# Kernel tuning notes

Measured on AMD Instinct MI355X. Metric: run time of the kernel, lower is better.

The kernel has to match this reference:

```python
import jax, jax.numpy as jnp
import numpy as np

B, H, W, C = 32, 56, 56, 128
HEADS, WS, SHIFT = 4, 7, 3
P = 10            # prompt_len = PERTASK_LEN(5) * n_tasks(2)
R = 4             # LoRA rank
HID = 512         # mlp hidden = 4*C
LORA_SCALE = 1.0
NW = (H // WS) * (W // WS)
NWIN = WS * WS


def _rel_pos_index():
    coords = np.stack(np.meshgrid(np.arange(WS), np.arange(WS), indexing='ij')).reshape(2, -1)
    rel = (coords[:, :, None] - coords[:, None, :]).transpose(1, 2, 0)
    rel[:, :, 0] += WS - 1
    rel[:, :, 1] += WS - 1
    rel[:, :, 0] *= 2 * WS - 1
    return rel.sum(-1)  # (49, 49)


def _attn_mask():
    img = np.zeros((H, W))
    cnt = 0
    for hs in (slice(0, -WS), slice(-WS, -SHIFT), slice(-SHIFT, None)):
        for ws_ in (slice(0, -WS), slice(-WS, -SHIFT), slice(-SHIFT, None)):
            img[hs, ws_] = cnt
            cnt += 1
    mw = img.reshape(H // WS, WS, W // WS, WS).transpose(0, 2, 1, 3).reshape(-1, NWIN)
    am = mw[:, None, :] - mw[:, :, None]
    return np.where(am != 0, -100.0, 0.0).astype(np.float32)  # (nW, 49, 49)

RPI = _rel_pos_index()
ATTN_MASK = jnp.asarray(_attn_mask())


def window_partition(x):  # (B,H,W,C) -> (B*nW, ws*ws, C)
    b = x.shape[0]
    x = x.reshape(b, H // WS, WS, W // WS, WS, C)
    return x.transpose(0, 1, 3, 2, 4, 5).reshape(-1, NWIN, C)


def window_reverse(w):  # (B*nW, ws*ws, C) -> (B,H,W,C)
    x = w.reshape(-1, H // WS, W // WS, WS, WS, C)
    return x.transpose(0, 1, 3, 2, 4, 5).reshape(-1, H, W, C)


def _ln(t, g, b):
    m = t.mean(-1, keepdims=True)
    v = ((t - m) ** 2).mean(-1, keepdims=True)
    return (t - m) / jnp.sqrt(v + 1e-5) * g + b


def _tal(t, w, b, la, lb):  # TAModuleLinear: base linear + shared LoRA branch
    return t @ w + b + (t @ la) @ lb * LORA_SCALE


def setup_inputs() -> dict:
    key = jax.random.key(0)
    ks = jax.random.split(key, 16)
    s = 0.02
    return {
        'x': jax.random.normal(ks[0], (B, H * W, C), jnp.float32),
        'spa_prompts': jax.random.normal(ks[1], (B, P, C), jnp.float32),
        'norm1_g': jnp.ones((C,), jnp.float32),
        'norm1_b': jnp.zeros((C,), jnp.float32),
        'qkv_w': jax.random.normal(ks[2], (C, 3 * C), jnp.float32) * s,
        'qkv_b': jnp.zeros((3 * C,), jnp.float32),
        'qkv_la': jax.random.normal(ks[3], (C, R), jnp.float32) * s,
        'qkv_lb': jax.random.normal(ks[4], (R, 3 * C), jnp.float32) * s,
        'rpb_table': jax.random.normal(ks[5], ((2 * WS - 1) ** 2, HEADS), jnp.float32) * s,
        'proj_w': jax.random.normal(ks[6], (C, C), jnp.float32) * s,
        'proj_b': jnp.zeros((C,), jnp.float32),
        'proj_la': jax.random.normal(ks[7], (C, R), jnp.float32) * s,
        'proj_lb': jax.random.normal(ks[8], (R, C), jnp.float32) * s,
        'norm2_g': jnp.ones((C,), jnp.float32),
        'norm2_b': jnp.zeros((C,), jnp.float32),
        'fc1_w': jax.random.normal(ks[9], (C, HID), jnp.float32) * s,
        'fc1_b': jnp.zeros((HID,), jnp.float32),
        'fc1_la': jax.random.normal(ks[10], (C, R), jnp.float32) * s,
        'fc1_lb': jax.random.normal(ks[11], (R, HID), jnp.float32) * s,
        'fc2_w': jax.random.normal(ks[12], (HID, C), jnp.float32) * s,
        'fc2_b': jnp.zeros((C,), jnp.float32),
        'fc2_la': jax.random.normal(ks[13], (HID, R), jnp.float32) * s,
        'fc2_lb': jax.random.normal(ks[14], (R, C), jnp.float32) * s,
    }


def reference(x, spa_prompts, norm1_g, norm1_b, qkv_w, qkv_b, qkv_la, qkv_lb,
              rpb_table, proj_w, proj_b, proj_la, proj_lb, norm2_g, norm2_b,
              fc1_w, fc1_b, fc1_la, fc1_lb, fc2_w, fc2_b, fc2_la, fc2_lb):
    d = C // HEADS
    qk_scale = d ** -0.5
    N = NWIN + P
    B_ = B * NW

    shortcut = x
    h = _ln(x, norm1_g, norm1_b).reshape(B, H, W, C)
    h = jnp.roll(h, shift=(-SHIFT, -SHIFT), axis=(1, 2))          # cyclic shift
    xw = window_partition(h)                                      # (B*nW, 49, C)

    # prepend shared spatial prompts to every window
    sp = jnp.broadcast_to(spa_prompts[:, None], (B, NW, P, C)).reshape(B_, P, C)
    t = jnp.concatenate([sp, xw], axis=1)                         # (B_, N, C)

    qkv = _tal(t, qkv_w, qkv_b, qkv_la, qkv_lb)
    qkv = qkv.reshape(B_, N, 3, HEADS, d).transpose(2, 0, 3, 1, 4)
    q, k, v = qkv[0], qkv[1], qkv[2]

    attn = jnp.einsum('bhnd,bhmd->bhnm', q, k) * qk_scale         # (B_, h, N, N)
    bias = rpb_table[RPI.reshape(-1)].reshape(NWIN, NWIN, HEADS).transpose(2, 0, 1)
    attn = attn.at[:, :, P:, P:].add(bias[None])
    attn = attn.reshape(B, NW, HEADS, N, N)
    attn = attn.at[:, :, :, P:, P:].add(ATTN_MASK[None, :, None]) # shifted-window mask
    attn = jax.nn.softmax(attn.reshape(B_, HEADS, N, N), axis=-1)

    out = jnp.einsum('bhnm,bhmd->bnhd', attn, v).reshape(B_, N, C)
    out = _tal(out, proj_w, proj_b, proj_la, proj_lb)

    out = out[:, P:]                                              # drop prompt tokens
    h = window_reverse(out)
    h = jnp.roll(h, shift=(SHIFT, SHIFT), axis=(1, 2)).reshape(B, H * W, C)
    x1 = shortcut + h                                             # attn residual

    m = _ln(x1, norm2_g, norm2_b)
    m = jax.nn.gelu(_tal(m, fc1_w, fc1_b, fc1_la, fc1_lb), approximate=False)
    m = _tal(m, fc2_w, fc2_b, fc2_la, fc2_lb)
    return x1 + m
```

## Files before the change

### kernel.cpp

```cpp
#include <hip/hip_runtime.h>

typedef unsigned short u16;
typedef unsigned int   u32;
typedef short bf16x8 __attribute__((ext_vector_type(8)));
typedef short bf16x4 __attribute__((ext_vector_type(4)));
typedef float f32x4  __attribute__((ext_vector_type(4)));

#define HIMG 56
#define WIMG 56
#define CH   128
#define NHEADS 4
#define WSZ  7
#define SSH  3
#define PP   10
#define HIDD 512
#define NWIN 49
#define NTOK 59
#define BWIN 2048
#define DH   32
#define MWIN 120832
#define MPIX 100352

__device__ __forceinline__ u16 f2b(float f) {
  u32 u = __float_as_uint(f);
  u += 0x7fffu + ((u >> 16) & 1u);
  return (u16)(u >> 16);
}
__device__ __forceinline__ u32 pack2(float a, float b) {
  return (u32)f2b(a) | ((u32)f2b(b) << 16);
}
__device__ __forceinline__ float gelu(float x) {
  const float z = fabsf(x) * 0.70710678118654752f;
  const float t = 1.0f / (1.0f + 0.3275911f * z);
  const float p = t * (0.254829592f + t * (-0.284496736f + t * (1.421413741f +
                  t * (-1.453152027f + t * 1.061405429f))));
  const float erfz = copysignf(1.0f - p * __expf(-z * z), x);
  return 0.5f * x * (1.0f + erfz);
}

__global__ void fuse_all_kernel(
    const float* __restrict__ qw,  const float* __restrict__ qa,  const float* __restrict__ qb,
    const float* __restrict__ pw,  const float* __restrict__ pa,  const float* __restrict__ pb,
    const float* __restrict__ f1w, const float* __restrict__ f1a, const float* __restrict__ f1b,
    const float* __restrict__ f2w, const float* __restrict__ f2a, const float* __restrict__ f2b2,
    u16* __restrict__ out)
{
  int idx = blockIdx.x * 256 + threadIdx.x;
  if (idx >= 196608) return;
  int n, k, Nc;
  const float *w, *la, *lb;
  if (idx < 49152) {
    const int li = idx;
    const int j = li & 7, lane = (li >> 3) & 63, kk = (li >> 9) & 3, c16 = li >> 11;
    n = c16 * 16 + (lane & 15);
    k = kk * 32 + (lane >> 4) * 8 + j;
    w = qw; la = qa; lb = qb; Nc = 384;
  } else if (idx < 65536) {
    const int li = idx - 49152;
    const int j = li & 7, lane = (li >> 3) & 63, kk = (li >> 9) & 3, c16 = li >> 11;
    n = c16 * 16 + (lane & 15);
    k = kk * 32 + (lane >> 4) * 8 + j;
    w = pw; la = pa; lb = pb; Nc = 128;
  } else if (idx < 131072) {
    const int li = idx - 65536;
    const int j = li & 7, lane = (li >> 3) & 63, kk = (li >> 9) & 3, c16 = li >> 11;
    n = c16 * 16 + (lane & 15);
    k = kk * 32 + (lane >> 4) * 8 + j;
    w = f1w; la = f1a; lb = f1b; Nc = 512;
  } else {
    const int li = idx - 131072;
    const int j = li & 7, lane = (li >> 3) & 63, kk2 = (li >> 9) & 1, hb = (li >> 10) & 7, o16 = li >> 13;
    n = o16 * 16 + (lane & 15);
    k = hb * 64 + kk2 * 32 + (lane >> 4) * 8 + j;
    w = f2w; la = f2a; lb = f2b2; Nc = 128;
  }
  float s = w[k * Nc + n];
  #pragma unroll
  for (int r = 0; r < 4; ++r) s += la[k * 4 + r] * lb[r * Nc + n];
  out[idx] = f2b(s);
}

__global__ void bm_kernel(const float* __restrict__ rpb, float* __restrict__ bm)
{
  const int idx = blockIdx.x * 256 + threadIdx.x;
  const int j = idx & 63, i = (idx >> 6) & 63, h = (idx >> 12) & 3, type = idx >> 14;
  float v = 0.f;
  if (i < 49) {
    if (j >= 59) v = -1e30f;
    else if (j >= PP) {
      const int jw = j - PP;
      const int ih = i / 7, iw = i - ih * 7, jh = jw / 7, jw2 = jw - jh * 7;
      v = rpb[((ih - jh + 6) * 13 + (iw - jw2 + 6)) * NHEADS + h];
      const int wh7 = type >> 1, ww7 = type & 1;
      const int mi = 3 * (wh7 ? (ih < 4 ? 1 : 2) : 0) + (ww7 ? (iw < 4 ? 1 : 2) : 0);
      const int mj = 3 * (wh7 ? (jh < 4 ? 1 : 2) : 0) + (ww7 ? (jw2 < 4 ? 1 : 2) : 0);
      if (mi != mj) v -= 100.f;
    }
  }
  bm[idx] = v;
}

__global__ __launch_bounds__(256) void ln1_gather_kernel(
    const float* __restrict__ x, const float* __restrict__ prompts,
    const float* __restrict__ g, const float* __restrict__ bb,
    u16* __restrict__ t)
{
  const int tok  = blockIdx.x * 4 + (threadIdx.x >> 6);
  const int lane = threadIdx.x & 63;
  const int b_ = tok / NTOK, n = tok - b_ * NTOK;
  u32* dst = (u32*)(t + (size_t)tok * CH) + lane;
  if (n < PP) {
    const int b = b_ >> 6;
    const float2 v = *(const float2*)(prompts + ((size_t)b * PP + n) * CH + lane * 2);
    *dst = pack2(v.x, v.y);
    return;
  }
  const int w  = b_ & 63;
  const int wi = n - PP;
  const int hr = (w >> 3) * WSZ + wi / WSZ;
  const int wc = (w & 7) * WSZ + wi % WSZ;
  const int hs  = (hr + SSH) % HIMG;
  const int ws2 = (wc + SSH) % WIMG;
  const float2 v = *(const float2*)(x + ((size_t)(b_ >> 6) * (HIMG * WIMG) + hs * WIMG + ws2) * CH + lane * 2);
  float s = v.x + v.y, s2 = v.x * v.x + v.y * v.y;
  #pragma unroll
  for (int o = 32; o > 0; o >>= 1) { s += __shfl_xor(s, o); s2 += __shfl_xor(s2, o); }
  const float mean = s * (1.0f / CH);
  const float inv  = rsqrtf(s2 * (1.0f / CH) - mean * mean + 1e-5f);
  const float2 gg = *(const float2*)(g  + lane * 2);
  const float2 bv = *(const float2*)(bb + lane * 2);
  *dst = pack2((v.x - mean) * inv * gg.x + bv.x, (v.y - mean) * inv * gg.y + bv.y);
}

#define QKS 136
#define VTS 72
#define PS  68
__global__ __launch_bounds__(256, 3) void qkv_attn_kernel(
    const u16* __restrict__ t, const u16* __restrict__ wqf,
    const float* __restrict__ qbias, const float* __restrict__ bm,
    u16* __restrict__ attn_out)
{
  __shared__ __align__(16) u16 smem[26624];
  u16* q_lds = smem;
  u16* k_lds = smem + 64 * QKS;
  u16* vt    = smem + 128 * QKS;
  u16* p_lds = smem;

  const int tid = threadIdx.x;
  const int wv = tid >> 6, lane = tid & 63;
  const int lr = lane & 15, lk = lane >> 4;
  const int b_ = blockIdx.x;
  const long tbase = (long)b_ * NTOK;

  bf16x8 af[4][4];
  #pragma unroll
  for (int mt = 0; mt < 4; ++mt) {
    int tok = mt * 16 + lr; if (tok > 58) tok = 58;
    #pragma unroll
    for (int kk = 0; kk < 4; ++kk)
      af[mt][kk] = *(const bf16x8*)(t + (tbase + tok) * CH + kk * 32 + lk * 8);
  }
  #pragma unroll
  for (int nf = 0; nf < 6; ++nf) {
    const int c = wv * 96 + nf * 16 + lr;
    const int sel = wv * 6 + nf;
    bf16x8 bw[4];
    #pragma unroll
    for (int kk = 0; kk < 4; ++kk)
      bw[kk] = *(const bf16x8*)(wqf + ((sel * 4 + kk) * 64 + lane) * 8);
    f32x4 a4[4];
    #pragma unroll
    for (int mt = 0; mt < 4; ++mt) a4[mt] = (f32x4){0.f, 0.f, 0.f, 0.f};
    #pragma unroll
    for (int kk = 0; kk < 4; ++kk)
      #pragma unroll
      for (int mt = 0; mt < 4; ++mt)
        a4[mt] = __builtin_amdgcn_mfma_f32_16x16x32_bf16(af[mt][kk], bw[kk], a4[mt], 0, 0, 0);
    const float bs = qbias[c];
    #pragma unroll
    for (int mt = 0; mt < 4; ++mt) {
      const int tok0 = mt * 16 + lk * 4;
      if (sel < 8) {
        #pragma unroll
        for (int rg = 0; rg < 4; ++rg)
          q_lds[(tok0 + rg) * QKS + c] = f2b(a4[mt][rg] + bs);
      } else if (sel < 16) {
        #pragma unroll
        for (int rg = 0; rg < 4; ++rg)
          k_lds[(tok0 + rg) * QKS + (c - 128)] = f2b(a4[mt][rg] + bs);
      } else {
        ushort4 pk = make_ushort4(f2b(a4[mt][0] + bs), f2b(a4[mt][1] + bs),
                                  f2b(a4[mt][2] + bs), f2b(a4[mt][3] + bs));
        *(ushort4*)&vt[(c - 256) * VTS + tok0] = pk;
      }
    }
  }
  __syncthreads();

  const int h = wv;
  const int w = b_ & 63;
  const int type = (((w >> 3) == 7) ? 2 : 0) + (((w & 7) == 7) ? 1 : 0);
  const float scale = 0.17677669529663687f;

  bf16x8 kf[4], qf[4];
  #pragma unroll
  for (int t4 = 0; t4 < 4; ++t4) {
    kf[t4] = *(const bf16x8*)&k_lds[(t4 * 16 + lr) * QKS + h * DH + lk * 8];
    int tq = PP + t4 * 16 + lr; if (tq > 63) tq = 63;
    qf[t4] = *(const bf16x8*)&q_lds[tq * QKS + h * DH + lk * 8];
  }
  f32x4 sacc[4][4];
  #pragma unroll
  for (int a = 0; a < 4; ++a)
    #pragma unroll
    for (int b = 0; b < 4; ++b)
      sacc[a][b] = (f32x4){0.f, 0.f, 0.f, 0.f};
  #pragma unroll
  for (int mtj = 0; mtj < 4; ++mtj)
    #pragma unroll
    for (int nti = 0; nti < 4; ++nti)
      sacc[mtj][nti] = __builtin_amdgcn_mfma_f32_16x16x32_bf16(kf[mtj], qf[nti], sacc[mtj][nti], 0, 0, 0);

  const float* bmh = bm + (size_t)(type * NHEADS + h) * 64 * 64;
  #pragma unroll
  for (int nti = 0; nti < 4; ++nti) {
    const int i = nti * 16 + lr;
    float sv[16];
    #pragma unroll
    for (int mtj = 0; mtj < 4; ++mtj) {
      const float4 bmv = *(const float4*)(bmh + i * 64 + mtj * 16 + lk * 4);
      sv[mtj * 4 + 0] = sacc[mtj][nti][0] * scale + bmv.x;
      sv[mtj * 4 + 1] = sacc[mtj][nti][1] * scale + bmv.y;
      sv[mtj * 4 + 2] = sacc[mtj][nti][2] * scale + bmv.z;
      sv[mtj * 4 + 3] = sacc[mtj][nti][3] * scale + bmv.w;
    }
    float mx = sv[0];
    #pragma unroll
    for (int q = 1; q < 16; ++q) mx = fmaxf(mx, sv[q]);
    mx = fmaxf(mx, __shfl_xor(mx, 16));
    mx = fmaxf(mx, __shfl_xor(mx, 32));
    float sum = 0.f;
    #pragma unroll
    for (int q = 0; q < 16; ++q) { sv[q] = __expf(sv[q] - mx); sum += sv[q]; }
    sum += __shfl_xor(sum, 16);
    sum += __shfl_xor(sum, 32);
    const float inv = 1.0f / sum;
    #pragma unroll
    for (int mtj = 0; mtj < 4; ++mtj) {
      sacc[mtj][nti][0] = sv[mtj * 4 + 0] * inv;
      sacc[mtj][nti][1] = sv[mtj * 4 + 1] * inv;
      sacc[mtj][nti][2] = sv[mtj * 4 + 2] * inv;
      sacc[mtj][nti][3] = sv[mtj * 4 + 3] * inv;
    }
  }
  __syncthreads();

  u16* ph = p_lds + h * 64 * PS;
  #pragma unroll
  for (int nti = 0; nti < 4; ++nti) {
    const int i = nti * 16 + lr;
    #pragma unroll
    for (int mtj = 0; mtj < 4; ++mtj) {
      const ushort4 pk = make_ushort4(f2b(sacc[mtj][nti][0]), f2b(sacc[mtj][nti][1]),
                                      f2b(sacc[mtj][nti][2]), f2b(sacc[mtj][nti][3]));
      *(ushort4*)&ph[i * PS + mtj * 16 + lk * 4] = pk;
    }
  }
  __syncthreads();

  f32x4 oacc[4][2];
  #pragma unroll
  for (int a = 0; a < 4; ++a) { oacc[a][0] = (f32x4){0,0,0,0}; oacc[a][1] = (f32x4){0,0,0,0}; }
  #pragma unroll
  for (int ks = 0; ks < 2; ++ks) {
    bf16x8 pa[4];
    #pragma unroll
    for (int mt = 0; mt < 4; ++mt) {
      const u16* pr = &ph[(mt * 16 + lr) * PS + ks * 32 + lk * 8];
      const bf16x4 lo = *(const bf16x4*)pr;
      const bf16x4 hi = *(const bf16x4*)(pr + 4);
      pa[mt] = __builtin_shufflevector(lo, hi, 0, 1, 2, 3, 4, 5, 6, 7);
    }
    bf16x8 bv[2];
    #pragma unroll
    for (int nd = 0; nd < 2; ++nd)
      bv[nd] = *(const bf16x8*)&vt[(h * DH + nd * 16 + lr) * VTS + ks * 32 + lk * 8];
    #pragma unroll
    for (int mt = 0; mt < 4; ++mt)
      #pragma unroll
      for (int nd = 0; nd < 2; ++nd)
        oacc[mt][nd] = __builtin_amdgcn_mfma_f32_16x16x32_bf16(pa[mt], bv[nd], oacc[mt][nd], 0, 0, 0);
  }

  #pragma unroll
  for (int mt = 0; mt < 4; ++mt)
    #pragma unroll
    for (int rg = 0; rg < 4; ++rg) {
      const int i = mt * 16 + lk * 4 + rg;
      ph[i * PS + lr]      = f2b(oacc[mt][0][rg]);
      ph[i * PS + 16 + lr] = f2b(oacc[mt][1][rg]);
    }
  __syncthreads();
  if (lane < NWIN) {
    const u16* src = &ph[lane * PS];
    u16* dst = attn_out + ((size_t)b_ * NWIN + lane) * CH + h * DH;
    #pragma unroll
    for (int c = 0; c < 8; ++c)
      *(uint2*)(dst + c * 4) = *(const uint2*)(src + c * 4);
  }
}

#define HS 68
__global__ __launch_bounds__(256, 4) void proj_mlp_kernel(
    const u16* __restrict__ ao, const u16* __restrict__ wprojf,
    const float* __restrict__ pbias, const float* __restrict__ x,
    const float* __restrict__ g2, const float* __restrict__ b2,
    const u16* __restrict__ w1f, const float* __restrict__ b1,
    const u16* __restrict__ w2f, const float* __restrict__ b2f,
    float* __restrict__ outp)
{
  __shared__ __align__(16) char smem[33792];
  u16*   sa  = (u16*)smem;
  float* T32 = (float*)smem;
  u16*   sm  = (u16*)(smem + 16896);
  u16*   H   = (u16*)(smem + 25088);
  const int tid = threadIdx.x;
  const int wv = tid >> 6, lane = tid & 63;
  const int lr = lane & 15, lk = lane >> 4;
  const long rowbase = (long)blockIdx.x * 32;

  #pragma unroll
  for (int it = 0; it < 2; ++it) {
    const int c = it * 256 + tid;
    const int r = c >> 4, s = c & 15;
    const int k8 = s ^ (r & 15);
    const int pix = (int)rowbase + r;
    const int b  = pix / 3136;
    const int rem = pix - b * 3136;
    const int hf = rem / 56, wf = rem - hf * 56;
    int hs = hf + 53; if (hs >= 56) hs -= 56;
    int ws2 = wf + 53; if (ws2 >= 56) ws2 -= 56;
    const int w  = (hs / 7) * 8 + (ws2 / 7);
    const int wi = (hs % 7) * 7 + (ws2 % 7);
    const long arow = ((long)b * 64 + w) * NWIN + wi;
    __builtin_amdgcn_global_load_lds((const void*)(ao + arow * CH + k8 * 8),
                                     (void*)(sa + c * 8), 16, 0, 0);
  }
  __syncthreads();

  f32x4 pacc[2][2];
  #pragma unroll
  for (int a = 0; a < 2; ++a) { pacc[a][0] = (f32x4){0,0,0,0}; pacc[a][1] = (f32x4){0,0,0,0}; }
  #pragma unroll
  for (int kk = 0; kk < 4; ++kk) {
    bf16x8 af[2];
    #pragma unroll
    for (int mt = 0; mt < 2; ++mt) {
      const int r = mt * 16 + lr;
      af[mt] = *(const bf16x8*)(sa + r * 128 + (((kk * 4 + lk) ^ (r & 15)) << 3));
    }
    #pragma unroll
    for (int nf = 0; nf < 2; ++nf) {
      const int c16 = wv * 2 + nf;
      const bf16x8 bw = *(const bf16x8*)(wprojf + ((c16 * 4 + kk) * 64 + lane) * 8);
      #pragma unroll
      for (int mt = 0; mt < 2; ++mt)
        pacc[mt][nf] = __builtin_amdgcn_mfma_f32_16x16x32_bf16(af[mt], bw, pacc[mt][nf], 0, 0, 0);
    }
  }
  __syncthreads();

  #pragma unroll
  for (int nf = 0; nf < 2; ++nf) {
    const int col = (wv * 2 + nf) * 16 + lr;
    const float bs = pbias[col];
    #pragma unroll
    for (int mt = 0; mt < 2; ++mt)
      #pragma unroll
      for (int j = 0; j < 4; ++j)
        T32[(mt * 16 + lk * 4 + j) * 132 + col] = pacc[mt][nf][j] + bs;
  }
  __syncthreads();
  const int rl = tid >> 3, q = tid & 7;
  float4 xv[4];
  float sum = 0.f, sq = 0.f;
  {
    const float* xrow = x + (rowbase + rl) * CH;
    #pragma unroll
    for (int i = 0; i < 4; ++i) {
      float4 tv = *(const float4*)&T32[rl * 132 + q * 4 + i * 32];
      const float4 xr = *(const float4*)(xrow + q * 4 + i * 32);
      tv.x += xr.x; tv.y += xr.y; tv.z += xr.z; tv.w += xr.w;
      xv[i] = tv;
      sum += tv.x + tv.y + tv.z + tv.w;
      sq  += tv.x * tv.x + tv.y * tv.y + tv.z * tv.z + tv.w * tv.w;
    }
  }
  sum += __shfl_xor(sum, 1); sq += __shfl_xor(sq, 1);
  sum += __shfl_xor(sum, 2); sq += __shfl_xor(sq, 2);
  sum += __shfl_xor(sum, 4); sq += __shfl_xor(sq, 4);
  {
    const float mean = sum * (1.0f / CH);
    const float inv  = rsqrtf(sq * (1.0f / CH) - mean * mean + 1e-5f);
    #pragma unroll
    for (int i = 0; i < 4; ++i) {
      const int col0 = q * 4 + i * 32;
      const float4 gg = *(const float4*)(g2 + col0);
      const float4 bb = *(const float4*)(b2 + col0);
      const float m0 = (xv[i].x - mean) * inv * gg.x + bb.x;
      const float m1 = (xv[i].y - mean) * inv * gg.y + bb.y;
      const float m2 = (xv[i].z - mean) * inv * gg.z + bb.z;
      const float m3 = (xv[i].w - mean) * inv * gg.w + bb.w;
      const int slot = col0 >> 3;
      const int off = rl * 128 + ((slot ^ (rl & 15)) << 3) + (col0 & 7);
      uint2 pk; pk.x = pack2(m0, m1); pk.y = pack2(m2, m3);
      *(uint2*)&sm[off] = pk;
    }
  }
  __syncthreads();

  f32x4 oad[2][2];
  #pragma unroll
  for (int a = 0; a < 2; ++a) { oad[a][0] = (f32x4){0,0,0,0}; oad[a][1] = (f32x4){0,0,0,0}; }

  auto stage1 = [&](int hb, u16* Hbuf) {
    f32x4 c1[2];
    c1[0] = (f32x4){0.f, 0.f, 0.f, 0.f};
    c1[1] = (f32x4){0.f, 0.f, 0.f, 0.f};
    #pragma unroll
    for (int kk = 0; kk < 4; ++kk) {
      const int c16 = hb * 4 + wv;
      const bf16x8 a1 = *(const bf16x8*)(w1f + ((c16 * 4 + kk) * 64 + lane) * 8);
      bf16x8 bmv[2];
      #pragma unroll
      for (int nt = 0; nt < 2; ++nt) {
        const int r = nt * 16 + lr;
        bmv[nt] = *(const bf16x8*)(sm + r * 128 + (((kk * 4 + lk) ^ (r & 15)) << 3));
      }
      c1[0] = __builtin_amdgcn_mfma_f32_16x16x32_bf16(a1, bmv[0], c1[0], 0, 0, 0);
      c1[1] = __builtin_amdgcn_mfma_f32_16x16x32_bf16(a1, bmv[1], c1[1], 0, 0, 0);
    }
    const int hc0 = wv * 16 + lk * 4;
    const float4 bs = *(const float4*)(b1 + hb * 64 + hc0);
    #pragma unroll
    for (int nt = 0; nt < 2; ++nt) {
      const int tok = nt * 16 + lr;
      const ushort4 pk = make_ushort4(
          f2b(gelu(c1[nt][0] + bs.x)), f2b(gelu(c1[nt][1] + bs.y)),
          f2b(gelu(c1[nt][2] + bs.z)), f2b(gelu(c1[nt][3] + bs.w)));
      *(ushort4*)&Hbuf[tok * HS + hc0] = pk;
    }
  };

  auto stage2 = [&](int hb, const u16* Hbuf) {
    #pragma unroll
    for (int kk2 = 0; kk2 < 2; ++kk2) {
      bf16x8 a2[2];
      #pragma unroll
      for (int mt = 0; mt < 2; ++mt) {
        const u16* pr = &Hbuf[(mt * 16 + lr) * HS + kk2 * 32 + lk * 8];
        const bf16x4 lo = *(const bf16x4*)pr;
        const bf16x4 hi = *(const bf16x4*)(pr + 4);
        a2[mt] = __builtin_shufflevector(lo, hi, 0, 1, 2, 3, 4, 5, 6, 7);
      }
      #pragma unroll
      for (int nf2 = 0; nf2 < 2; ++nf2) {
        const int o16 = wv * 2 + nf2;
        const bf16x8 bw = *(const bf16x8*)(w2f + (((o16 * 8 + hb) * 2 + kk2) * 64 + lane) * 8);
        #pragma unroll
        for (int mt = 0; mt < 2; ++mt)
          oad[mt][nf2] = __builtin_amdgcn_mfma_f32_16x16x32_bf16(a2[mt], bw, oad[mt][nf2], 0, 0, 0);
      }
    }
  };

  u16* H0 = H;
  u16* H1 = H + 32 * HS;
  stage1(0, H0);
  __syncthreads();
  for (int hb = 0; hb < 8; ++hb) {
    u16* cur = (hb & 1) ? H1 : H0;
    u16* nxt = (hb & 1) ? H0 : H1;
    if (hb < 7) stage1(hb + 1, nxt);
    stage2(hb, cur);
    __syncthreads();
  }

  #pragma unroll
  for (int nf2 = 0; nf2 < 2; ++nf2) {
    const int col = wv * 32 + nf2 * 16 + lr;
    const float bs = b2f[col];
    #pragma unroll
    for (int mt = 0; mt < 2; ++mt)
      #pragma unroll
      for (int j = 0; j < 4; ++j)
        T32[(mt * 16 + lk * 4 + j) * 132 + col] = oad[mt][nf2][j] + bs;
  }
  __syncthreads();
  {
    float* orow = outp + (rowbase + rl) * CH;
    #pragma unroll
    for (int i = 0; i < 4; ++i) {
      float4 v = *(const float4*)&T32[rl * 132 + q * 4 + i * 32];
      v.x += xv[i].x; v.y += xv[i].y; v.z += xv[i].z; v.w += xv[i].w;
      *(float4*)(orow + q * 4 + i * 32) = v;
    }
  }
}

extern "C" void kernel_launch(void* const* d_in, const int* in_sizes, int n_in,
                              void* d_out, int out_size, void* d_ws, size_t ws_size,
                              hipStream_t stream)
{
  const float* x       = (const float*)d_in[0];
  const float* prompts = (const float*)d_in[1];
  const float* n1g     = (const float*)d_in[2];
  const float* n1b     = (const float*)d_in[3];
  const float* qkv_w   = (const float*)d_in[4];
  const float* qkv_b   = (const float*)d_in[5];
  const float* qkv_la  = (const float*)d_in[6];
  const float* qkv_lb  = (const float*)d_in[7];
  const float* rpb     = (const float*)d_in[8];
  const float* proj_w  = (const float*)d_in[9];
  const float* proj_b  = (const float*)d_in[10];
  const float* proj_la = (const float*)d_in[11];
  const float* proj_lb = (const float*)d_in[12];
  const float* n2g     = (const float*)d_in[13];
  const float* n2b     = (const float*)d_in[14];
  const float* fc1_w   = (const float*)d_in[15];
  const float* fc1_b   = (const float*)d_in[16];
  const float* fc1_la  = (const float*)d_in[17];
  const float* fc1_lb  = (const float*)d_in[18];
  const float* fc2_w   = (const float*)d_in[19];
  const float* fc2_b   = (const float*)d_in[20];
  const float* fc2_la  = (const float*)d_in[21];
  const float* fc2_lb  = (const float*)d_in[22];

  char* ws = (char*)d_ws;
  u16* wT     = (u16*)ws;
  u16* wqf    = wT;
  u16* wprojf = wT + 49152;
  u16* w1f    = wT + 65536;
  u16* w2f    = wT + 131072;
  float* bm   = (float*)(ws + 393216);
  char* p = ws + 393216 + 262144;
  u16* tbuf  = (u16*)p;                       p += (size_t)MWIN * CH * 2;
  u16* aobuf = (u16*)p;

  fuse_all_kernel<<<768, 256, 0, stream>>>(
      qkv_w, qkv_la, qkv_lb, proj_w, proj_la, proj_lb,
      fc1_w, fc1_la, fc1_lb, fc2_w, fc2_la, fc2_lb, wT);

  bm_kernel<<<256, 256, 0, stream>>>(rpb, bm);

  ln1_gather_kernel<<<MWIN / 4, 256, 0, stream>>>(x, prompts, n1g, n1b, tbuf);

  qkv_attn_kernel<<<BWIN, 256, 0, stream>>>(tbuf, wqf, qkv_b, bm, aobuf);

  proj_mlp_kernel<<<MPIX / 32, 256, 0, stream>>>(
      aobuf, wprojf, proj_b, x, n2g, n2b,
      w1f, fc1_b, w2f, fc2_b, (float*)d_out);
}
```

Measured before the change: 160.6 us.

## Fuse LN1 gather into qkv-attention kernel and shrink proj-MLP shared memory

Drops the separate LN1/shift/window-gather kernel. The qkv_attn kernel now loads fp32 x and the prompts directly, computes layernorm in registers and packs bf16 A fragments, which removes a round trip of the token buffer through global memory. Separately, proj_mlp stores the projection output as bf16 instead of fp32 and aliases the LN2 buffer onto that space. This cuts LDS from 33792 to 17408 bytes and raises launch bounds to 8 blocks per SM. The price is an extra sync, possible register pressure, redundant x reads across the four waves, and an extra bf16 rounding of the attention residual.

```diff
diff --git a/kernel.cpp b/kernel.cpp
--- a/kernel.cpp
+++ b/kernel.cpp
@@ -29,6 +29,7 @@
 __device__ __forceinline__ u32 pack2(float a, float b) {
   return (u32)f2b(a) | ((u32)f2b(b) << 16);
 }
+__device__ __forceinline__ float bfh2f(u16 h) { return __uint_as_float((u32)h << 16); }
 __device__ __forceinline__ float gelu(float x) {
   const float z = fabsf(x) * 0.70710678118654752f;
   const float t = 1.0f / (1.0f + 0.3275911f * z);
@@ -100,45 +101,14 @@
   bm[idx] = v;
 }
 
-__global__ __launch_bounds__(256) void ln1_gather_kernel(
-    const float* __restrict__ x, const float* __restrict__ prompts,
-    const float* __restrict__ g, const float* __restrict__ bb,
-    u16* __restrict__ t)
-{
-  const int tok  = blockIdx.x * 4 + (threadIdx.x >> 6);
-  const int lane = threadIdx.x & 63;
-  const int b_ = tok / NTOK, n = tok - b_ * NTOK;
-  u32* dst = (u32*)(t + (size_t)tok * CH) + lane;
-  if (n < PP) {
-    const int b = b_ >> 6;
-    const float2 v = *(const float2*)(prompts + ((size_t)b * PP + n) * CH + lane * 2);
-    *dst = pack2(v.x, v.y);
-    return;
-  }
-  const int w  = b_ & 63;
-  const int wi = n - PP;
-  const int hr = (w >> 3) * WSZ + wi / WSZ;
-  const int wc = (w & 7) * WSZ + wi % WSZ;
-  const int hs  = (hr + SSH) % HIMG;
-  const int ws2 = (wc + SSH) % WIMG;
-  const float2 v = *(const float2*)(x + ((size_t)(b_ >> 6) * (HIMG * WIMG) + hs * WIMG + ws2) * CH + lane * 2);
-  float s = v.x + v.y, s2 = v.x * v.x + v.y * v.y;
-  #pragma unroll
-  for (int o = 32; o > 0; o >>= 1) { s += __shfl_xor(s, o); s2 += __shfl_xor(s2, o); }
-  const float mean = s * (1.0f / CH);
-  const float inv  = rsqrtf(s2 * (1.0f / CH) - mean * mean + 1e-5f);
-  const float2 gg = *(const float2*)(g  + lane * 2);
-  const float2 bv = *(const float2*)(bb + lane * 2);
-  *dst = pack2((v.x - mean) * inv * gg.x + bv.x, (v.y - mean) * inv * gg.y + bv.y);
-}
-
 #define QKS 136
 #define VTS 72
 #define PS  68
 __global__ __launch_bounds__(256, 3) void qkv_attn_kernel(
-    const u16* __restrict__ t, const u16* __restrict__ wqf,
-    const float* __restrict__ qbias, const float* __restrict__ bm,
-    u16* __restrict__ attn_out)
+    const float* __restrict__ x, const float* __restrict__ prompts,
+    const float* __restrict__ n1g, const float* __restrict__ n1b,
+    const u16* __restrict__ wqf, const float* __restrict__ qbias,
+    const float* __restrict__ bm, u16* __restrict__ attn_out)
 {
   __shared__ __align__(16) u16 smem[26624];
   u16* q_lds = smem;
@@ -150,16 +120,64 @@
   const int wv = tid >> 6, lane = tid & 63;
   const int lr = lane & 15, lk = lane >> 4;
   const int b_ = blockIdx.x;
-  const long tbase = (long)b_ * NTOK;
+  const int bimg = b_ >> 6;
+  const int wwin = b_ & 63;
 
   bf16x8 af[4][4];
   #pragma unroll
   for (int mt = 0; mt < 4; ++mt) {
-    int tok = mt * 16 + lr; if (tok > 58) tok = 58;
-    #pragma unroll
-    for (int kk = 0; kk < 4; ++kk)
-      af[mt][kk] = *(const bf16x8*)(t + (tbase + tok) * CH + kk * 32 + lk * 8);
-  }
+    int n = mt * 16 + lr; if (n > 58) n = 58;
+    const float* src;
+    if (n < PP) {
+      src = prompts + ((size_t)bimg * PP + n) * CH;
+    } else {
+      const int wi = n - PP;
+      const int hr = (wwin >> 3) * WSZ + wi / WSZ;
+      const int wc = (wwin & 7) * WSZ + wi % WSZ;
+      const int hs = (hr + SSH) % HIMG;
+      const int ws2 = (wc + SSH) % WIMG;
+      src = x + ((size_t)bimg * (HIMG * WIMG) + hs * WIMG + ws2) * CH;
+    }
+    float4 va[8];
+    #pragma unroll
+    for (int kk = 0; kk < 4; ++kk) {
+      va[kk * 2]     = *(const float4*)(src + kk * 32 + lk * 8);
+      va[kk * 2 + 1] = *(const float4*)(src + kk * 32 + lk * 8 + 4);
+    }
+    float s = 0.f, s2 = 0.f;
+    #pragma unroll
+    for (int p = 0; p < 8; ++p) {
+      s  += va[p].x + va[p].y + va[p].z + va[p].w;
+      s2 += va[p].x * va[p].x + va[p].y * va[p].y + va[p].z * va[p].z + va[p].w * va[p].w;
+    }
+    s  += __shfl_xor(s, 16);  s2 += __shfl_xor(s2, 16);
+    s  += __shfl_xor(s, 32);  s2 += __shfl_xor(s2, 32);
+    const float mean = s * (1.0f / CH);
+    const float inv  = rsqrtf(s2 * (1.0f / CH) - mean * mean + 1e-5f);
+    const bool doln = (n >= PP);
+    #pragma unroll
+    for (int kk = 0; kk < 4; ++kk) {
+      const int c0 = kk * 32 + lk * 8;
+      const float4 g0 = *(const float4*)(n1g + c0);
+      const float4 g1 = *(const float4*)(n1g + c0 + 4);
+      const float4 bb0 = *(const float4*)(n1b + c0);
+      const float4 bb1 = *(const float4*)(n1b + c0 + 4);
+      const float4 A = va[kk * 2], B = va[kk * 2 + 1];
+      float o0 = doln ? (A.x - mean) * inv * g0.x + bb0.x : A.x;
+      float o1 = doln ? (A.y - mean) * inv * g0.y + bb0.y : A.y;
+      float o2 = doln ? (A.z - mean) * inv * g0.z + bb0.z : A.z;
+      float o3 = doln ? (A.w - mean) * inv * g0.w + bb0.w : A.w;
+      float o4 = doln ? (B.x - mean) * inv * g1.x + bb1.x : B.x;
+      float o5 = doln ? (B.y - mean) * inv * g1.y + bb1.y : B.y;
+      float o6 = doln ? (B.z - mean) * inv * g1.z + bb1.z : B.z;
+      float o7 = doln ? (B.w - mean) * inv * g1.w + bb1.w : B.w;
+      uint4 pk;
+      pk.x = pack2(o0, o1); pk.y = pack2(o2, o3);
+      pk.z = pack2(o4, o5); pk.w = pack2(o6, o7);
+      af[mt][kk] = *(bf16x8*)&pk;
+    }
+  }
+
   #pragma unroll
   for (int nf = 0; nf < 6; ++nf) {
     const int c = wv * 96 + nf * 16 + lr;
@@ -198,8 +216,7 @@
   __syncthreads();
 
   const int h = wv;
-  const int w = b_ & 63;
-  const int type = (((w >> 3) == 7) ? 2 : 0) + (((w & 7) == 7) ? 1 : 0);
+  const int type = (((wwin >> 3) == 7) ? 2 : 0) + (((wwin & 7) == 7) ? 1 : 0);
   const float scale = 0.17677669529663687f;
 
   bf16x8 kf[4], qf[4];
@@ -311,19 +328,20 @@
 }
 
 #define HS 68
-__global__ __launch_bounds__(256, 4) void proj_mlp_kernel(
+__global__ __launch_bounds__(256, 8) void proj_mlp_kernel(
     const u16* __restrict__ ao, const u16* __restrict__ wprojf,
     const float* __restrict__ pbias, const float* __restrict__ x,
     const float* __restrict__ g2, const float* __restrict__ b2,
     const u16* __restrict__ w1f, const float* __restrict__ b1,
-    const u16* __restrict__ w2f, const float* __restrict__ b2f,
+    const u16* __restrict__ w2f, const float* __restrict__ fc2b,
     float* __restrict__ outp)
 {
-  __shared__ __align__(16) char smem[33792];
+  __shared__ __align__(16) char smem[17408];
   u16*   sa  = (u16*)smem;
-  float* T32 = (float*)smem;
-  u16*   sm  = (u16*)(smem + 16896);
-  u16*   H   = (u16*)(smem + 25088);
+  u16*   T16 = (u16*)smem;
+  u16*   sm  = (u16*)smem;
+  u16*   H   = (u16*)(smem + 8704);
+  float* T32E = (float*)smem;
   const int tid = threadIdx.x;
   const int wv = tid >> 6, lane = tid & 63;
   const int lr = lane & 15, lk = lane >> 4;
@@ -378,9 +396,10 @@
     for (int mt = 0; mt < 2; ++mt)
       #pragma unroll
       for (int j = 0; j < 4; ++j)
-        T32[(mt * 16 + lk * 4 + j) * 132 + col] = pacc[mt][nf][j] + bs;
-  }
-  __syncthreads();
+        T16[(mt * 16 + lk * 4 + j) * 136 + col] = f2b(pacc[mt][nf][j] + bs);
+  }
+  __syncthreads();
+
   const int rl = tid >> 3, q = tid & 7;
   float4 xv[4];
   float sum = 0.f, sq = 0.f;
@@ -388,9 +407,11 @@
     const float* xrow = x + (rowbase + rl) * CH;
     #pragma unroll
     for (int i = 0; i < 4; ++i) {
-      float4 tv = *(const float4*)&T32[rl * 132 + q * 4 + i * 32];
+      const ushort4 hv = *(const ushort4*)&T16[rl * 136 + q * 4 + i * 32];
       const float4 xr = *(const float4*)(xrow + q * 4 + i * 32);
-      tv.x += xr.x; tv.y += xr.y; tv.z += xr.z; tv.w += xr.w;
+      float4 tv;
+      tv.x = bfh2f(hv.x) + xr.x; tv.y = bfh2f(hv.y) + xr.y;
+      tv.z = bfh2f(hv.z) + xr.z; tv.w = bfh2f(hv.w) + xr.w;
       xv[i] = tv;
       sum += tv.x + tv.y + tv.z + tv.w;
       sq  += tv.x * tv.x + tv.y * tv.y + tv.z * tv.z + tv.w * tv.w;
@@ -399,6 +420,7 @@
   sum += __shfl_xor(sum, 1); sq += __shfl_xor(sq, 1);
   sum += __shfl_xor(sum, 2); sq += __shfl_xor(sq, 2);
   sum += __shfl_xor(sum, 4); sq += __shfl_xor(sq, 4);
+  uint2 mreg[4];
   {
     const float mean = sum * (1.0f / CH);
     const float inv  = rsqrtf(sq * (1.0f / CH) - mean * mean + 1e-5f);
@@ -407,15 +429,20 @@
       const int col0 = q * 4 + i * 32;
       const float4 gg = *(const float4*)(g2 + col0);
       const float4 bb = *(const float4*)(b2 + col0);
-      const float m0 = (xv[i].x - mean) * inv * gg.x + bb.x;
-      const float m1 = (xv[i].y - mean) * inv * gg.y + bb.y;
-      const float m2 = (xv[i].z - mean) * inv * gg.z + bb.z;
-      const float m3 = (xv[i].w - mean) * inv * gg.w + bb.w;
-      const int slot = col0 >> 3;
-      const int off = rl * 128 + ((slot ^ (rl & 15)) << 3) + (col0 & 7);
-      uint2 pk; pk.x = pack2(m0, m1); pk.y = pack2(m2, m3);
-      *(uint2*)&sm[off] = pk;
-    }
+      mreg[i].x = pack2((xv[i].x - mean) * inv * gg.x + bb.x,
+                        (xv[i].y - mean) * inv * gg.y + bb.y);
+      mreg[i].y = pack2((xv[i].z - mean) * inv * gg.z + bb.z,
+                        (xv[i].w - mean) * inv * gg.w + bb.w);
+    }
+  }
+  __syncthreads();
+
+  #pragma unroll
+  for (int i = 0; i < 4; ++i) {
+    const int col0 = q * 4 + i * 32;
+    const int slot = col0 >> 3;
+    const int off = rl * 128 + ((slot ^ (rl & 15)) << 3) + (col0 & 7);
+    *(uint2*)&sm[off] = mreg[i];
   }
   __syncthreads();
 
@@ -489,19 +516,19 @@
   #pragma unroll
   for (int nf2 = 0; nf2 < 2; ++nf2) {
     const int col = wv * 32 + nf2 * 16 + lr;
-    const float bs = b2f[col];
+    const float bs = fc2b[col];
     #pragma unroll
     for (int mt = 0; mt < 2; ++mt)
       #pragma unroll
       for (int j = 0; j < 4; ++j)
-        T32[(mt * 16 + lk * 4 + j) * 132 + col] = oad[mt][nf2][j] + bs;
+        T32E[(mt * 16 + lk * 4 + j) * 132 + col] = oad[mt][nf2][j] + bs;
   }
   __syncthreads();
   {
     float* orow = outp + (rowbase + rl) * CH;
     #pragma unroll
     for (int i = 0; i < 4; ++i) {
-      float4 v = *(const float4*)&T32[rl * 132 + q * 4 + i * 32];
+      float4 v = *(const float4*)&T32E[rl * 132 + q * 4 + i * 32];
       v.x += xv[i].x; v.y += xv[i].y; v.z += xv[i].z; v.w += xv[i].w;
       *(float4*)(orow + q * 4 + i * 32) = v;
     }
@@ -543,9 +570,7 @@
   u16* w1f    = wT + 65536;
   u16* w2f    = wT + 131072;
   float* bm   = (float*)(ws + 393216);
-  char* p = ws + 393216 + 262144;
-  u16* tbuf  = (u16*)p;                       p += (size_t)MWIN * CH * 2;
-  u16* aobuf = (u16*)p;
+  u16* aobuf  = (u16*)(ws + 393216 + 262144);
 
   fuse_all_kernel<<<768, 256, 0, stream>>>(
       qkv_w, qkv_la, qkv_lb, proj_w, proj_la, proj_lb,
@@ -553,9 +578,8 @@
 
   bm_kernel<<<256, 256, 0, stream>>>(rpb, bm);
 
-  ln1_gather_kernel<<<MWIN / 4, 256, 0, stream>>>(x, prompts, n1g, n1b, tbuf);
-
-  qkv_attn_kernel<<<BWIN, 256, 0, stream>>>(tbuf, wqf, qkv_b, bm, aobuf);
+  qkv_attn_kernel<<<BWIN, 256, 0, stream>>>(
+      x, prompts, n1g, n1b, wqf, qkv_b, bm, aobuf);
 
   proj_mlp_kernel<<<MPIX / 32, 256, 0, stream>>>(
       aobuf, wprojf, proj_b, x, n2g, n2b,
```

Measured after the change: 218.6 us. 36.1% more time.

## Fuse LN1 window gather into the QKV-attention kernel via swizzled LDS staging

Applied to the files above, without the earlier changes.

Removes the separate ln1_gather kernel and its bf16 token buffer in global memory. Each attention block now gathers its window's shifted pixels and prompts, applies LayerNorm and writes bf16 into an XOR-swizzled LDS region (reusing the V-transpose area) before loading the MFMA A fragments. This removes a global write and read of roughly 31MB and one kernel launch. In exchange it adds a sync and serial per-wave gather latency at the start of the attention kernel.

```diff
diff --git a/kernel.cpp b/kernel.cpp
--- a/kernel.cpp
+++ b/kernel.cpp
@@ -18,7 +18,6 @@
 #define NTOK 59
 #define BWIN 2048
 #define DH   32
-#define MWIN 120832
 #define MPIX 100352
 
 __device__ __forceinline__ u16 f2b(float f) {
@@ -100,66 +99,76 @@
   bm[idx] = v;
 }
 
-__global__ __launch_bounds__(256) void ln1_gather_kernel(
-    const float* __restrict__ x, const float* __restrict__ prompts,
-    const float* __restrict__ g, const float* __restrict__ bb,
-    u16* __restrict__ t)
-{
-  const int tok  = blockIdx.x * 4 + (threadIdx.x >> 6);
-  const int lane = threadIdx.x & 63;
-  const int b_ = tok / NTOK, n = tok - b_ * NTOK;
-  u32* dst = (u32*)(t + (size_t)tok * CH) + lane;
-  if (n < PP) {
-    const int b = b_ >> 6;
-    const float2 v = *(const float2*)(prompts + ((size_t)b * PP + n) * CH + lane * 2);
-    *dst = pack2(v.x, v.y);
-    return;
-  }
-  const int w  = b_ & 63;
-  const int wi = n - PP;
-  const int hr = (w >> 3) * WSZ + wi / WSZ;
-  const int wc = (w & 7) * WSZ + wi % WSZ;
-  const int hs  = (hr + SSH) % HIMG;
-  const int ws2 = (wc + SSH) % WIMG;
-  const float2 v = *(const float2*)(x + ((size_t)(b_ >> 6) * (HIMG * WIMG) + hs * WIMG + ws2) * CH + lane * 2);
-  float s = v.x + v.y, s2 = v.x * v.x + v.y * v.y;
-  #pragma unroll
-  for (int o = 32; o > 0; o >>= 1) { s += __shfl_xor(s, o); s2 += __shfl_xor(s2, o); }
-  const float mean = s * (1.0f / CH);
-  const float inv  = rsqrtf(s2 * (1.0f / CH) - mean * mean + 1e-5f);
-  const float2 gg = *(const float2*)(g  + lane * 2);
-  const float2 bv = *(const float2*)(bb + lane * 2);
-  *dst = pack2((v.x - mean) * inv * gg.x + bv.x, (v.y - mean) * inv * gg.y + bv.y);
-}
-
 #define QKS 136
 #define VTS 72
 #define PS  68
 __global__ __launch_bounds__(256, 3) void qkv_attn_kernel(
-    const u16* __restrict__ t, const u16* __restrict__ wqf,
-    const float* __restrict__ qbias, const float* __restrict__ bm,
-    u16* __restrict__ attn_out)
+    const float* __restrict__ x, const float* __restrict__ prompts,
+    const float* __restrict__ n1g, const float* __restrict__ n1b,
+    const u16* __restrict__ wqf, const float* __restrict__ qbias,
+    const float* __restrict__ bm, u16* __restrict__ attn_out)
 {
   __shared__ __align__(16) u16 smem[26624];
   u16* q_lds = smem;
   u16* k_lds = smem + 64 * QKS;
   u16* vt    = smem + 128 * QKS;
   u16* p_lds = smem;
+  char* t_lds = (char*)vt;
 
   const int tid = threadIdx.x;
   const int wv = tid >> 6, lane = tid & 63;
   const int lr = lane & 15, lk = lane >> 4;
   const int b_ = blockIdx.x;
-  const long tbase = (long)b_ * NTOK;
+  const int bimg = b_ >> 6;
+  const int wwin = b_ & 63;
+
+  {
+    const float2 gg = *(const float2*)(n1g + lane * 2);
+    const float2 bv = *(const float2*)(n1b + lane * 2);
+    for (int it = 0; it < 16; ++it) {
+      const int n = wv * 16 + it;
+      if (n >= NTOK) break;
+      const float* src;
+      if (n < PP) {
+        src = prompts + ((size_t)bimg * PP + n) * CH;
+      } else {
+        const int wi = n - PP;
+        const int hr = (wwin >> 3) * WSZ + wi / WSZ;
+        const int wc = (wwin & 7) * WSZ + wi % WSZ;
+        const int hs = (hr + SSH) % HIMG;
+        const int ws2 = (wc + SSH) % WIMG;
+        src = x + ((size_t)bimg * (HIMG * WIMG) + hs * WIMG + ws2) * CH;
+      }
+      const float2 v = *(const float2*)(src + lane * 2);
+      u32 pk;
+      if (n < PP) {
+        pk = pack2(v.x, v.y);
+      } else {
+        float s = v.x + v.y, s2 = v.x * v.x + v.y * v.y;
+        #pragma unroll
+        for (int o = 32; o > 0; o >>= 1) { s += __shfl_xor(s, o); s2 += __shfl_xor(s2, o); }
+        const float mean = s * (1.0f / CH);
+        const float inv  = rsqrtf(s2 * (1.0f / CH) - mean * mean + 1e-5f);
+        pk = pack2((v.x - mean) * inv * gg.x + bv.x, (v.y - mean) * inv * gg.y + bv.y);
+      }
+      const int slot = (lane >> 2) ^ (n & 7);
+      *(u32*)(t_lds + n * 256 + slot * 16 + (lane & 3) * 4) = pk;
+    }
+  }
+  __syncthreads();
 
   bf16x8 af[4][4];
   #pragma unroll
   for (int mt = 0; mt < 4; ++mt) {
     int tok = mt * 16 + lr; if (tok > 58) tok = 58;
     #pragma unroll
-    for (int kk = 0; kk < 4; ++kk)
-      af[mt][kk] = *(const bf16x8*)(t + (tbase + tok) * CH + kk * 32 + lk * 8);
-  }
+    for (int kk = 0; kk < 4; ++kk) {
+      const int slot = (kk * 4 + lk) ^ (tok & 7);
+      af[mt][kk] = *(const bf16x8*)(t_lds + tok * 256 + slot * 16);
+    }
+  }
+  __syncthreads();
+
   #pragma unroll
   for (int nf = 0; nf < 6; ++nf) {
     const int c = wv * 96 + nf * 16 + lr;
@@ -198,8 +207,7 @@
   __syncthreads();
 
   const int h = wv;
-  const int w = b_ & 63;
-  const int type = (((w >> 3) == 7) ? 2 : 0) + (((w & 7) == 7) ? 1 : 0);
+  const int type = (((wwin >> 3) == 7) ? 2 : 0) + (((wwin & 7) == 7) ? 1 : 0);
   const float scale = 0.17677669529663687f;
 
   bf16x8 kf[4], qf[4];
@@ -316,7 +324,7 @@
     const float* __restrict__ pbias, const float* __restrict__ x,
     const float* __restrict__ g2, const float* __restrict__ b2,
     const u16* __restrict__ w1f, const float* __restrict__ b1,
-    const u16* __restrict__ w2f, const float* __restrict__ b2f,
+    const u16* __restrict__ w2f, const float* __restrict__ fc2b,
     float* __restrict__ outp)
 {
   __shared__ __align__(16) char smem[33792];
@@ -489,7 +497,7 @@
   #pragma unroll
   for (int nf2 = 0; nf2 < 2; ++nf2) {
     const int col = wv * 32 + nf2 * 16 + lr;
-    const float bs = b2f[col];
+    const float bs = fc2b[col];
     #pragma unroll
     for (int mt = 0; mt < 2; ++mt)
       #pragma unroll
@@ -543,9 +551,7 @@
   u16* w1f    = wT + 65536;
   u16* w2f    = wT + 131072;
   float* bm   = (float*)(ws + 393216);
-  char* p = ws + 393216 + 262144;
-  u16* tbuf  = (u16*)p;                       p += (size_t)MWIN * CH * 2;
-  u16* aobuf = (u16*)p;
+  u16* aobuf  = (u16*)(ws + 393216 + 262144);
 
   fuse_all_kernel<<<768, 256, 0, stream>>>(
       qkv_w, qkv_la, qkv_lb, proj_w, proj_la, proj_lb,
@@ -553,9 +559,8 @@
 
   bm_kernel<<<256, 256, 0, stream>>>(rpb, bm);
 
-  ln1_gather_kernel<<<MWIN / 4, 256, 0, stream>>>(x, prompts, n1g, n1b, tbuf);
-
-  qkv_attn_kernel<<<BWIN, 256, 0, stream>>>(tbuf, wqf, qkv_b, bm, aobuf);
+  qkv_attn_kernel<<<BWIN, 256, 0, stream>>>(
+      x, prompts, n1g, n1b, wqf, qkv_b, bm, aobuf);
 
   proj_mlp_kernel<<<MPIX / 32, 256, 0, stream>>>(
       aobuf, wprojf, proj_b, x, n2g, n2b,
```

After: 157.3 us. -2.1%, faster.
